# Kernel tuning notes

Measured on AMD Instinct MI355X. Metric: run time of the kernel, lower is better.

The kernel has to match this reference:

```python
import jax, jax.numpy as jnp
import numpy as np

D_MODEL = 1024
NUM_HEADS = 16
D_K = D_MODEL // NUM_HEADS  # 64
B, T = 2, 2048


def rope_tables(seq_len, d_k):
    # Matches RotaryPositionalEmbedding + the slice apply_rotary takes:
    # only cos/sin of freqs (dim d_k//2) are used.
    half = d_k // 2
    inv_freq = 1.0 / (10000.0 ** (jnp.arange(0, d_k, 2, dtype=jnp.float32) / d_k))  # (half,)
    t = jnp.arange(seq_len, dtype=jnp.float32)
    freqs = jnp.einsum('i,j->ij', t, inv_freq)  # (T, half)
    return jnp.cos(freqs), jnp.sin(freqs)


def apply_rotary(x, cos, sin):
    # x: (B, H, T, D); rotate first 2*half dims as two halves
    half = x.shape[-1] // 2
    x1, x2 = x[..., :half], x[..., half:2 * half]
    c = cos[None, None, :x.shape[2], :half]
    s = sin[None, None, :x.shape[2], :half]
    return jnp.concatenate([x1 * c - x2 * s, x1 * s + x2 * c], axis=-1)


def setup_inputs() -> dict:
    key = jax.random.key(0)
    ks = jax.random.split(key, 5)
    scale = 1.0 / np.sqrt(D_MODEL)
    return {
        'x': jax.random.normal(ks[0], (B, T, D_MODEL), dtype=jnp.float32),
        'wq': jax.random.normal(ks[1], (D_MODEL, D_MODEL), dtype=jnp.float32) * scale,
        'wk': jax.random.normal(ks[2], (D_MODEL, D_MODEL), dtype=jnp.float32) * scale,
        'wv': jax.random.normal(ks[3], (D_MODEL, D_MODEL), dtype=jnp.float32) * scale,
        'wo': jax.random.normal(ks[4], (D_MODEL, D_MODEL), dtype=jnp.float32) * scale,
    }


def reference(x, wq, wk, wv, wo):
    Bs, Ts, _ = x.shape
    def proj(w):
        # nn.Linear: x @ w.T, then split heads -> (B, H, T, d_k)
        return (x @ w.T).reshape(Bs, Ts, NUM_HEADS, D_K).transpose(0, 2, 1, 3)
    Q, K, V = proj(wq), proj(wk), proj(wv)
    cos, sin = rope_tables(Ts, D_K)
    Q = apply_rotary(Q, cos, sin)
    K = apply_rotary(K, cos, sin)
    scores = jnp.einsum('bhqd,bhkd->bhqk', Q, K) / jnp.sqrt(jnp.float32(D_K))
    attn = jax.nn.softmax(scores, axis=-1)  # dropout is identity in eval
    out = jnp.einsum('bhqk,bhkd->bhqd', attn, V)
    out = out.transpose(0, 2, 1, 3).reshape(Bs, Ts, D_MODEL)
    return out @ wo.T
```

## Files before the change

kernel.cpp:

```cpp
#include <hip/hip_runtime.h>
#include <math.h>

typedef __attribute__((ext_vector_type(8))) short short8;
typedef __attribute__((ext_vector_type(4))) short short4v;
typedef __attribute__((ext_vector_type(4))) float f32x4;
typedef __attribute__((ext_vector_type(16))) float f32x16;

#define D_MODEL 1024
#define NUM_HEADS 16
#define D_K 64
#define B_SZ 2
#define T_SZ 2048
#define M_ROWS (B_SZ * T_SZ)
#define LSTR 72
#define LOG2E 1.4426950408889634f
#define KVSPLIT 1024

__device__ __forceinline__ unsigned short f2bf(float f) {
    union { float f; unsigned int u; } v; v.f = f;
    unsigned int r = v.u + 0x7FFF + ((v.u >> 16) & 1);
    return (unsigned short)(r >> 16);
}
__device__ __forceinline__ void gload_lds16(const void* g, void* l) {
    __builtin_amdgcn_global_load_lds(
        (const __attribute__((address_space(1))) unsigned int*)g,
        (__attribute__((address_space(3))) unsigned int*)l, 16, 0, 0);
}
__device__ __forceinline__ int cvtpk(float lo, float hi) {
    int r;
    asm("v_cvt_pk_bf16_f32 %0, %1, %2" : "=v"(r) : "v"(lo), "v"(hi));
    return r;
}
__device__ __forceinline__ float fast_exp2(float x) {
#if __has_builtin(__builtin_amdgcn_exp2f)
    return __builtin_amdgcn_exp2f(x);
#else
    float r; asm("v_exp_f32 %0, %1" : "=v"(r) : "v"(x)); return r;
#endif
}

__global__ __launch_bounds__(256) void cvt_all(
    const float* __restrict__ x,  const float* __restrict__ w0,
    const float* __restrict__ w1, const float* __restrict__ w2,
    const float* __restrict__ w3, unsigned short* __restrict__ dst)
{
    const size_t NX8 = (size_t)M_ROWS * D_MODEL / 8;
    const size_t NW8 = (size_t)D_MODEL * D_MODEL / 8;
    size_t i = (size_t)blockIdx.x * 256 + threadIdx.x;
    const float* src; size_t off;
    if (i < NX8) { src = x; off = i; }
    else {
        size_t j = i - NX8;
        int ws = (int)(j >> 17);
        off = j & (NW8 - 1);
        src = (ws == 0) ? w0 : (ws == 1) ? w1 : (ws == 2) ? w2 : w3;
    }
    const float4* p = (const float4*)src + 2 * off;
    float4 a = p[0], b = p[1];
    short8 o;
    o[0] = f2bf(a.x); o[1] = f2bf(a.y); o[2] = f2bf(a.z); o[3] = f2bf(a.w);
    o[4] = f2bf(b.x); o[5] = f2bf(b.y); o[6] = f2bf(b.z); o[7] = f2bf(b.w);
    *((short8*)dst + i) = o;
}

__global__ __launch_bounds__(256) void rope_table(float2* __restrict__ tab)
{
    int idx = blockIdx.x * 256 + threadIdx.x;
    int t = idx >> 5, i = idx & 31;
    const float invf = (float)pow(10000.0, -(double)i / 32.0);
    float s, c;
    sincosf((float)t * invf, &s, &c);
    tab[idx] = make_float2(c, s);
}

__global__ __launch_bounds__(256) void gemm_qkv(
    const unsigned short* __restrict__ Xb,
    const unsigned short* __restrict__ Wq,
    const unsigned short* __restrict__ Wk,
    const unsigned short* __restrict__ Wv,
    unsigned short* __restrict__ Qb,
    unsigned short* __restrict__ Kb,
    unsigned short* __restrict__ Vtg,
    const float2* __restrict__ tab)
{
    const int z = blockIdx.z;
    const unsigned short* W = (z == 0) ? Wq : (z == 1) ? Wk : Wv;

    __shared__ unsigned short Als[128 * 32];
    __shared__ unsigned short Bls[128 * 32];

    const int tid = threadIdx.x;
    const int lane = tid & 63, wid = tid >> 6;
    const int g = lane >> 4, c16 = lane & 15;
    const int wr = wid >> 1, wc = wid & 1;
    const int m0 = blockIdx.y * 128, n0 = blockIdx.x * 128;

    const int sr = tid >> 2, sc = (tid & 3) * 8;
    const unsigned short* xg = Xb + (size_t)(m0 + sr) * D_MODEL + sc;
    const unsigned short* wg = W + (size_t)(n0 + sr) * D_MODEL + sc;
    unsigned short* adst = Als + wid * 512;
    unsigned short* bdst = Bls + wid * 512;

    f32x4 acc[4][4] = {};

    for (int k0 = 0; k0 < D_MODEL; k0 += 32) {
        __syncthreads();
        gload_lds16(xg + k0, adst);
        gload_lds16(xg + k0 + (size_t)64 * D_MODEL, adst + 2048);
        gload_lds16(wg + k0, bdst);
        gload_lds16(wg + k0 + (size_t)64 * D_MODEL, bdst + 2048);
        __syncthreads();
        short8 af[4], bf[4];
#pragma unroll
        for (int mf = 0; mf < 4; mf++)
            af[mf] = *(const short8*)&Als[(wr * 64 + mf * 16 + c16) * 32 + g * 8];
#pragma unroll
        for (int nf = 0; nf < 4; nf++)
            bf[nf] = *(const short8*)&Bls[(wc * 64 + nf * 16 + c16) * 32 + g * 8];
#pragma unroll
        for (int mf = 0; mf < 4; mf++)
#pragma unroll
            for (int nf = 0; nf < 4; nf++)
                acc[mf][nf] = __builtin_amdgcn_mfma_f32_16x16x32_bf16(
                    af[mf], bf[nf], acc[mf][nf], 0, 0, 0);
    }

    if (z < 2) {
        const float qs = (z == 0) ? 0.125f * LOG2E : 1.0f;
        unsigned short* Y = (z == 0) ? Qb : Kb;
#pragma unroll
        for (int mf = 0; mf < 4; mf++)
#pragma unroll
            for (int j = 0; j < 4; j++) {
                int row = m0 + wr * 64 + mf * 16 + g * 4 + j;
                int t = row & (T_SZ - 1);
#pragma unroll
                for (int nf = 0; nf < 2; nf++) {
                    float2 cs = tab[t * 32 + nf * 16 + c16];
                    float a = acc[mf][nf][j], b2 = acc[mf][nf + 2][j];
                    acc[mf][nf][j]     = (a * cs.x - b2 * cs.y) * qs;
                    acc[mf][nf + 2][j] = (a * cs.y + b2 * cs.x) * qs;
                }
            }
#pragma unroll
        for (int mf = 0; mf < 4; mf++)
#pragma unroll
            for (int nf = 0; nf < 4; nf++)
#pragma unroll
                for (int j = 0; j < 4; j++) {
                    int row = m0 + wr * 64 + mf * 16 + g * 4 + j;
                    int col = n0 + wc * 64 + nf * 16 + c16;
                    Y[(size_t)row * D_MODEL + col] = f2bf(acc[mf][nf][j]);
                }
    } else {
#pragma unroll
        for (int mf = 0; mf < 4; mf++) {
            int row0 = m0 + wr * 64 + mf * 16 + g * 4;
            int bq = row0 >> 11;
            int t0 = row0 & (T_SZ - 1);
#pragma unroll
            for (int nf = 0; nf < 4; nf++) {
                int col = n0 + wc * 64 + nf * 16 + c16;
                int h = col >> 6, d = col & 63;
                short4v pk;
#pragma unroll
                for (int j = 0; j < 4; j++) pk[j] = (short)f2bf(acc[mf][nf][j]);
                *(short4v*)&Vtg[(size_t)((bq * 16 + h) * 64 + d) * T_SZ + t0] = pk;
            }
        }
    }
}

__global__ __launch_bounds__(256) void gemm_out(
    const unsigned short* __restrict__ Xb,
    const unsigned short* __restrict__ W,
    float* __restrict__ Y)
{
    __shared__ unsigned short Als[128 * 32];
    __shared__ unsigned short Bls[64 * 32];

    const int tid = threadIdx.x;
    const int lane = tid & 63, wid = tid >> 6;
    const int g = lane >> 4, c16 = lane & 15;
    const int wr = wid >> 1, wc = wid & 1;
    const int m0 = blockIdx.y * 128, n0 = blockIdx.x * 64;

    const int sr = tid >> 2, sc = (tid & 3) * 8;
    const unsigned short* xg = Xb + (size_t)(m0 + sr) * D_MODEL + sc;
    const unsigned short* wg = W + (size_t)(n0 + sr) * D_MODEL + sc;
    unsigned short* adst = Als + wid * 512;
    unsigned short* bdst = Bls + wid * 512;

    f32x4 acc[4][2] = {};

    for (int k0 = 0; k0 < D_MODEL; k0 += 32) {
        __syncthreads();
        gload_lds16(xg + k0, adst);
        gload_lds16(xg + k0 + (size_t)64 * D_MODEL, adst + 2048);
        gload_lds16(wg + k0, bdst);
        __syncthreads();
        short8 af[4], bf[2];
#pragma unroll
        for (int mf = 0; mf < 4; mf++)
            af[mf] = *(const short8*)&Als[(wr * 64 + mf * 16 + c16) * 32 + g * 8];
#pragma unroll
        for (int nf = 0; nf < 2; nf++)
            bf[nf] = *(const short8*)&Bls[(wc * 32 + nf * 16 + c16) * 32 + g * 8];
#pragma unroll
        for (int mf = 0; mf < 4; mf++)
#pragma unroll
            for (int nf = 0; nf < 2; nf++)
                acc[mf][nf] = __builtin_amdgcn_mfma_f32_16x16x32_bf16(
                    af[mf], bf[nf], acc[mf][nf], 0, 0, 0);
    }

#pragma unroll
    for (int mf = 0; mf < 4; mf++)
#pragma unroll
        for (int nf = 0; nf < 2; nf++)
#pragma unroll
            for (int j = 0; j < 4; j++) {
                int row = m0 + wr * 64 + mf * 16 + g * 4 + j;
                int col = n0 + wc * 32 + nf * 16 + c16;
                Y[(size_t)row * D_MODEL + col] = acc[mf][nf][j];
            }
}

#define PVAL(i) ((i) < 16 ? s0[(i) & 15] : s1[(i) & 15])

__global__ __launch_bounds__(512, 4) void attn_mfma32(
    const unsigned short* __restrict__ Qb,
    const unsigned short* __restrict__ Kb,
    const unsigned short* __restrict__ Vtg,
    unsigned short* __restrict__ Ob)
{
    __shared__ __align__(16) char smem[36864];

    const int tid = threadIdx.x;
    const int lane = tid & 63, wid = tid >> 6;
    const int kz = wid >> 2, wq = wid & 3;
    const int q32 = lane & 31, hi = lane >> 5;
    const int bh = blockIdx.y, b = bh >> 4, h = bh & (NUM_HEADS - 1);
    const int q0 = blockIdx.x * 128 + wq * 32;

    unsigned short* Ks = (unsigned short*)(smem + kz * 18432);
    unsigned short* Vt = Ks + 64 * LSTR;

    short8 qf[4];
    {
        const unsigned short* qsrc =
            Qb + (size_t)(b * T_SZ + q0 + q32) * D_MODEL + h * D_K + 8 * hi;
#pragma unroll
        for (int s = 0; s < 4; s++) qf[s] = *(const short8*)(qsrc + 16 * s);
    }

    f32x16 oacc0 = {}, oacc1 = {};
    float l = 0.f;

    const int t256 = tid & 255;
    const int krow = t256 >> 2, kcb = t256 & 3;
    const unsigned short* kbase =
        Kb + (size_t)(b * T_SZ + kz * KVSPLIT) * D_MODEL + h * D_K;
    const unsigned short* vtbase =
        Vtg + (size_t)((b * 16 + h) * 64) * T_SZ + kz * KVSPLIT;

    short8 pk0, pk1, pv0, pv1;
#define LOAD_KV(KT) do { \
    const unsigned short* _s = kbase + (size_t)((KT) + krow) * D_MODEL + kcb * 16; \
    pk0 = *(const short8*)_s; pk1 = *(const short8*)(_s + 8); \
    const unsigned short* _v = vtbase + (size_t)krow * T_SZ + (KT) + kcb * 16; \
    pv0 = *(const short8*)_v; pv1 = *(const short8*)(_v + 8); \
  } while (0)

    LOAD_KV(0);

    for (int kt = 0; kt < KVSPLIT; kt += 64) {
        __builtin_amdgcn_sched_barrier(0);
        __builtin_amdgcn_s_barrier();
        __builtin_amdgcn_sched_barrier(0);
        *(short8*)&Ks[krow * LSTR + kcb * 16] = pk0;
        *(short8*)&Ks[krow * LSTR + kcb * 16 + 8] = pk1;
        *(short8*)&Vt[krow * LSTR + kcb * 16] = pv0;
        *(short8*)&Vt[krow * LSTR + kcb * 16 + 8] = pv1;
        if (kt + 64 < KVSPLIT) LOAD_KV(kt + 64);
        asm volatile("s_waitcnt lgkmcnt(0)" ::: "memory");
        __builtin_amdgcn_s_barrier();
        __builtin_amdgcn_sched_barrier(0);

        f32x16 s0 = {}, s1 = {};
        __builtin_amdgcn_s_setprio(1);
#pragma unroll
        for (int s = 0; s < 4; s++) {
            short8 ak0 = *(const short8*)&Ks[q32 * LSTR + 16 * s + 8 * hi];
            short8 ak1 = *(const short8*)&Ks[(32 + q32) * LSTR + 16 * s + 8 * hi];
            s0 = __builtin_amdgcn_mfma_f32_32x32x16_bf16(ak0, qf[s], s0, 0, 0, 0);
            s1 = __builtin_amdgcn_mfma_f32_32x32x16_bf16(ak1, qf[s], s1, 0, 0, 0);
        }
        __builtin_amdgcn_s_setprio(0);

        float ps = 0.f;
#pragma unroll
        for (int r = 0; r < 16; r++) s0[r] = fast_exp2(s0[r]);
#pragma unroll
        for (int r = 0; r < 16; r++) s1[r] = fast_exp2(s1[r]);
#pragma unroll
        for (int r = 0; r < 16; r++) ps += s0[r] + s1[r];
        l += ps;

        __builtin_amdgcn_s_setprio(1);
#pragma unroll
        for (int t = 0; t < 4; t++) {
            const int b0 = 4 * ((2 * t + 0) & 3) + 16 * (t >> 1);
            const int b1 = 4 * ((2 * t + 1) & 3) + 16 * (t >> 1);
            int X0 = cvtpk(PVAL(b0), PVAL(b0 + 1));
            int X1 = cvtpk(PVAL(b0 + 2), PVAL(b0 + 3));
            int Y0 = cvtpk(PVAL(b1), PVAL(b1 + 1));
            int Y1 = cvtpk(PVAL(b1 + 2), PVAL(b1 + 3));
            asm("v_permlane32_swap_b32 %0, %1" : "+v"(X0), "+v"(Y0));
            asm("v_permlane32_swap_b32 %0, %1" : "+v"(X1), "+v"(Y1));
            union { int w[4]; short8 v; } af;
            af.w[0] = X0; af.w[1] = X1; af.w[2] = Y0; af.w[3] = Y1;
            short8 bv0 = *(const short8*)&Vt[q32 * LSTR + 16 * t + 8 * hi];
            short8 bv1 = *(const short8*)&Vt[(32 + q32) * LSTR + 16 * t + 8 * hi];
            oacc0 = __builtin_amdgcn_mfma_f32_32x32x16_bf16(af.v, bv0, oacc0, 0, 0, 0);
            oacc1 = __builtin_amdgcn_mfma_f32_32x32x16_bf16(af.v, bv1, oacc1, 0, 0, 0);
        }
        __builtin_amdgcn_s_setprio(0);
    }

    l += __shfl_xor(l, 32);

    __syncthreads();
    float* cmbO = (float*)smem;
    float* lb   = (float*)(smem + 32768);
    if (kz == 1) {
        if (hi == 0) lb[wq * 32 + q32] = l;
#pragma unroll
        for (int r = 0; r < 16; r++) {
            int qr = (r & 3) + 8 * (r >> 2) + 4 * hi;
            cmbO[wq * 2048 + qr * 64 + q32]      = oacc0[r];
            cmbO[wq * 2048 + qr * 64 + 32 + q32] = oacc1[r];
        }
    }
    __syncthreads();
    if (kz == 0) {
        float linv = 1.f / (l + lb[wq * 32 + q32]);
#pragma unroll
        for (int r = 0; r < 16; r++) {
            int qr = (r & 3) + 8 * (r >> 2) + 4 * hi;
            float iv = __shfl(linv, qr);
            float o0 = (oacc0[r] + cmbO[wq * 2048 + qr * 64 + q32]) * iv;
            float o1 = (oacc1[r] + cmbO[wq * 2048 + qr * 64 + 32 + q32]) * iv;
            size_t row = (size_t)(b * T_SZ + q0 + qr);
            Ob[row * D_MODEL + h * D_K + q32]      = f2bf(o0);
            Ob[row * D_MODEL + h * D_K + 32 + q32] = f2bf(o1);
        }
    }
}

extern "C" void kernel_launch(void* const* d_in, const int* in_sizes, int n_in,
                              void* d_out, int out_size, void* d_ws, size_t ws_size,
                              hipStream_t stream)
{
    const float* x  = (const float*)d_in[0];
    const float* wq = (const float*)d_in[1];
    const float* wk = (const float*)d_in[2];
    const float* wv = (const float*)d_in[3];
    const float* wo = (const float*)d_in[4];
    float* out = (float*)d_out;

    const size_t NX = (size_t)M_ROWS * D_MODEL;
    const size_t NW = (size_t)D_MODEL * D_MODEL;
    unsigned short* xb  = (unsigned short*)d_ws;
    unsigned short* wqb = xb + NX;
    unsigned short* wkb = wqb + NW;
    unsigned short* wvb = wkb + NW;
    unsigned short* wob = wvb + NW;
    unsigned short* Qb  = wob + NW;
    unsigned short* Kb  = Qb + NX;
    unsigned short* Vtg = Kb + NX;
    unsigned short* Ob  = Vtg + NX;
    float2* tab = (float2*)(Ob + NX);

    const int ncvt8 = (int)((NX + 4 * NW) / 8);
    cvt_all<<<dim3(ncvt8 / 256), dim3(256), 0, stream>>>(x, wq, wk, wv, wo, xb);
    rope_table<<<dim3(T_SZ * 32 / 256), dim3(256), 0, stream>>>(tab);

    gemm_qkv<<<dim3(D_MODEL / 128, M_ROWS / 128, 3), dim3(256), 0, stream>>>(
        xb, wqb, wkb, wvb, Qb, Kb, Vtg, tab);

    attn_mfma32<<<dim3(T_SZ / 128, B_SZ * NUM_HEADS), dim3(512), 0, stream>>>(
        Qb, Kb, Vtg, Ob);

    gemm_out<<<dim3(D_MODEL / 64, M_ROWS / 128), dim3(256), 0, stream>>>(Ob, wob, out);
}
```

Baseline: 200.7 us.

## Deepen GEMM K-tiles to 64 with XOR-swizzled LDS and block swizzle

```diff
diff --git a/kernel.cpp b/kernel.cpp
--- a/kernel.cpp
+++ b/kernel.cpp
@@ -75,54 +75,60 @@
 
 __global__ __launch_bounds__(256) void gemm_qkv(
     const unsigned short* __restrict__ Xb,
-    const unsigned short* __restrict__ Wq,
-    const unsigned short* __restrict__ Wk,
-    const unsigned short* __restrict__ Wv,
+    const unsigned short* __restrict__ Wb,
     unsigned short* __restrict__ Qb,
     unsigned short* __restrict__ Kb,
     unsigned short* __restrict__ Vtg,
     const float2* __restrict__ tab)
 {
-    const int z = blockIdx.z;
-    const unsigned short* W = (z == 0) ? Wq : (z == 1) ? Wk : Wv;
-
-    __shared__ unsigned short Als[128 * 32];
-    __shared__ unsigned short Bls[128 * 32];
+    __shared__ unsigned short Als[128 * 64];
+    __shared__ unsigned short Bls[128 * 64];
 
     const int tid = threadIdx.x;
     const int lane = tid & 63, wid = tid >> 6;
     const int g = lane >> 4, c16 = lane & 15;
     const int wr = wid >> 1, wc = wid & 1;
-    const int m0 = blockIdx.y * 128, n0 = blockIdx.x * 128;
-
-    const int sr = tid >> 2, sc = (tid & 3) * 8;
-    const unsigned short* xg = Xb + (size_t)(m0 + sr) * D_MODEL + sc;
-    const unsigned short* wg = W + (size_t)(n0 + sr) * D_MODEL + sc;
-    unsigned short* adst = Als + wid * 512;
-    unsigned short* bdst = Bls + wid * 512;
+
+    const int bid = blockIdx.x;
+    const int swz = (bid & 7) * 96 + (bid >> 3);
+    const int bm = swz / 24, bn = swz % 24;
+    const int m0 = bm * 128, n0p = bn * 128;
+    const int z = n0p >> 10, n0c = n0p & 1023;
+
+    const int l8 = lane >> 3, l7 = lane & 7;
+    const int scol = 8 * (l7 ^ l8);
+    const unsigned short* xsrc = Xb + (size_t)(m0 + wid * 32 + l8) * D_MODEL + scol;
+    const unsigned short* wsrc = Wb + (size_t)(n0p + wid * 32 + l8) * D_MODEL + scol;
 
     f32x4 acc[4][4] = {};
 
-    for (int k0 = 0; k0 < D_MODEL; k0 += 32) {
+    for (int k0 = 0; k0 < D_MODEL; k0 += 64) {
         __syncthreads();
-        gload_lds16(xg + k0, adst);
-        gload_lds16(xg + k0 + (size_t)64 * D_MODEL, adst + 2048);
-        gload_lds16(wg + k0, bdst);
-        gload_lds16(wg + k0 + (size_t)64 * D_MODEL, bdst + 2048);
+#pragma unroll
+        for (int i = 0; i < 4; i++) {
+            gload_lds16(xsrc + (size_t)i * 8 * D_MODEL + k0, Als + (wid * 32 + i * 8) * 64);
+            gload_lds16(wsrc + (size_t)i * 8 * D_MODEL + k0, Bls + (wid * 32 + i * 8) * 64);
+        }
         __syncthreads();
-        short8 af[4], bf[4];
-#pragma unroll
-        for (int mf = 0; mf < 4; mf++)
-            af[mf] = *(const short8*)&Als[(wr * 64 + mf * 16 + c16) * 32 + g * 8];
-#pragma unroll
-        for (int nf = 0; nf < 4; nf++)
-            bf[nf] = *(const short8*)&Bls[(wc * 64 + nf * 16 + c16) * 32 + g * 8];
-#pragma unroll
-        for (int mf = 0; mf < 4; mf++)
+#pragma unroll
+        for (int kk = 0; kk < 64; kk += 32) {
+            short8 af[4], bf[4];
+            const int sw = (c16 & 7) * 8;
+#pragma unroll
+            for (int mf = 0; mf < 4; mf++)
+                af[mf] = *(const short8*)&Als[(wr * 64 + mf * 16 + c16) * 64 +
+                                              ((kk + g * 8) ^ sw)];
 #pragma unroll
             for (int nf = 0; nf < 4; nf++)
-                acc[mf][nf] = __builtin_amdgcn_mfma_f32_16x16x32_bf16(
-                    af[mf], bf[nf], acc[mf][nf], 0, 0, 0);
+                bf[nf] = *(const short8*)&Bls[(wc * 64 + nf * 16 + c16) * 64 +
+                                              ((kk + g * 8) ^ sw)];
+#pragma unroll
+            for (int mf = 0; mf < 4; mf++)
+#pragma unroll
+                for (int nf = 0; nf < 4; nf++)
+                    acc[mf][nf] = __builtin_amdgcn_mfma_f32_16x16x32_bf16(
+                        af[mf], bf[nf], acc[mf][nf], 0, 0, 0);
+        }
     }
 
     if (z < 2) {
@@ -149,7 +155,7 @@
 #pragma unroll
                 for (int j = 0; j < 4; j++) {
                     int row = m0 + wr * 64 + mf * 16 + g * 4 + j;
-                    int col = n0 + wc * 64 + nf * 16 + c16;
+                    int col = n0c + wc * 64 + nf * 16 + c16;
                     Y[(size_t)row * D_MODEL + col] = f2bf(acc[mf][nf][j]);
                 }
     } else {
@@ -160,7 +166,7 @@
             int t0 = row0 & (T_SZ - 1);
 #pragma unroll
             for (int nf = 0; nf < 4; nf++) {
-                int col = n0 + wc * 64 + nf * 16 + c16;
+                int col = n0c + wc * 64 + nf * 16 + c16;
                 int h = col >> 6, d = col & 63;
                 short4v pk;
 #pragma unroll
@@ -176,8 +182,8 @@
     const unsigned short* __restrict__ W,
     float* __restrict__ Y)
 {
-    __shared__ unsigned short Als[128 * 32];
-    __shared__ unsigned short Bls[64 * 32];
+    __shared__ unsigned short Als[128 * 64];
+    __shared__ unsigned short Bls[64 * 64];
 
     const int tid = threadIdx.x;
     const int lane = tid & 63, wid = tid >> 6;
@@ -185,33 +191,41 @@
     const int wr = wid >> 1, wc = wid & 1;
     const int m0 = blockIdx.y * 128, n0 = blockIdx.x * 64;
 
-    const int sr = tid >> 2, sc = (tid & 3) * 8;
-    const unsigned short* xg = Xb + (size_t)(m0 + sr) * D_MODEL + sc;
-    const unsigned short* wg = W + (size_t)(n0 + sr) * D_MODEL + sc;
-    unsigned short* adst = Als + wid * 512;
-    unsigned short* bdst = Bls + wid * 512;
+    const int l8 = lane >> 3, l7 = lane & 7;
+    const int scol = 8 * (l7 ^ l8);
+    const unsigned short* xsrc = Xb + (size_t)(m0 + wid * 32 + l8) * D_MODEL + scol;
+    const unsigned short* wsrc = W + (size_t)(n0 + wid * 16 + l8) * D_MODEL + scol;
 
     f32x4 acc[4][2] = {};
 
-    for (int k0 = 0; k0 < D_MODEL; k0 += 32) {
+    for (int k0 = 0; k0 < D_MODEL; k0 += 64) {
         __syncthreads();
-        gload_lds16(xg + k0, adst);
-        gload_lds16(xg + k0 + (size_t)64 * D_MODEL, adst + 2048);
-        gload_lds16(wg + k0, bdst);
+#pragma unroll
+        for (int i = 0; i < 4; i++)
+            gload_lds16(xsrc + (size_t)i * 8 * D_MODEL + k0, Als + (wid * 32 + i * 8) * 64);
+#pragma unroll
+        for (int j = 0; j < 2; j++)
+            gload_lds16(wsrc + (size_t)j * 8 * D_MODEL + k0, Bls + (wid * 16 + j * 8) * 64);
         __syncthreads();
-        short8 af[4], bf[2];
-#pragma unroll
-        for (int mf = 0; mf < 4; mf++)
-            af[mf] = *(const short8*)&Als[(wr * 64 + mf * 16 + c16) * 32 + g * 8];
-#pragma unroll
-        for (int nf = 0; nf < 2; nf++)
-            bf[nf] = *(const short8*)&Bls[(wc * 32 + nf * 16 + c16) * 32 + g * 8];
-#pragma unroll
-        for (int mf = 0; mf < 4; mf++)
+#pragma unroll
+        for (int kk = 0; kk < 64; kk += 32) {
+            short8 af[4], bf[2];
+            const int sw = (c16 & 7) * 8;
+#pragma unroll
+            for (int mf = 0; mf < 4; mf++)
+                af[mf] = *(const short8*)&Als[(wr * 64 + mf * 16 + c16) * 64 +
+                                              ((kk + g * 8) ^ sw)];
 #pragma unroll
             for (int nf = 0; nf < 2; nf++)
-                acc[mf][nf] = __builtin_amdgcn_mfma_f32_16x16x32_bf16(
-                    af[mf], bf[nf], acc[mf][nf], 0, 0, 0);
+                bf[nf] = *(const short8*)&Bls[(wc * 32 + nf * 16 + c16) * 64 +
+                                              ((kk + g * 8) ^ sw)];
+#pragma unroll
+            for (int mf = 0; mf < 4; mf++)
+#pragma unroll
+                for (int nf = 0; nf < 2; nf++)
+                    acc[mf][nf] = __builtin_amdgcn_mfma_f32_16x16x32_bf16(
+                        af[mf], bf[nf], acc[mf][nf], 0, 0, 0);
+        }
     }
 
 #pragma unroll
@@ -386,8 +400,7 @@
     cvt_all<<<dim3(ncvt8 / 256), dim3(256), 0, stream>>>(x, wq, wk, wv, wo, xb);
     rope_table<<<dim3(T_SZ * 32 / 256), dim3(256), 0, stream>>>(tab);
 
-    gemm_qkv<<<dim3(D_MODEL / 128, M_ROWS / 128, 3), dim3(256), 0, stream>>>(
-        xb, wqb, wkb, wvb, Qb, Kb, Vtg, tab);
+    gemm_qkv<<<dim3(768), dim3(256), 0, stream>>>(xb, wqb, Qb, Kb, Vtg, tab);
 
     attn_mfma32<<<dim3(T_SZ / 128, B_SZ * NUM_HEADS), dim3(512), 0, stream>>>(
         Qb, Kb, Vtg, Ob);
```

After: 190.4 us. 1.05x faster.
